# Optimization experiments

Hardware: AMD Instinct MI355X
Metric: run time of the kernel (lower is better)

## Reference

```python
import jax, jax.numpy as jnp
import numpy as np

B, D_IN = 8192, 4096
H1, H2, LAT = 2048, 1024, 256
NQ, NL = 16, 2


def setup_inputs() -> dict:
    key = jax.random.key(0)
    ks = jax.random.split(key, 16)
    def lin(k, fan_in, fan_out):
        k1, k2 = jax.random.split(k)
        s = 1.0 / np.sqrt(fan_in)
        W = jax.random.uniform(k1, (fan_out, fan_in), jnp.float32, -s, s)
        b = jax.random.uniform(k2, (fan_out,), jnp.float32, -s, s)
        return W, b
    x = jax.random.normal(ks[0], (B, D_IN), jnp.float32)
    We1, be1 = lin(ks[1], D_IN, H1)
    We2, be2 = lin(ks[2], H1, H2)
    We3, be3 = lin(ks[3], H2, LAT)
    P = jax.random.normal(ks[4], (NL, NQ, 3), jnp.float32)  # ansatz params (rx,ry,rz)
    Wd1, bd1 = lin(ks[5], NQ, H2)
    Wd2, bd2 = lin(ks[6], H2, H1)
    Wd3, bd3 = lin(ks[7], H1, D_IN)
    return {"x": x, "We1": We1, "be1": be1, "We2": We2, "be2": be2,
            "We3": We3, "be3": be3, "P": P, "Wd1": Wd1, "bd1": bd1,
            "Wd2": Wd2, "bd2": bd2, "Wd3": Wd3, "bd3": bd3}


def _quantum_block(latent, P):
    """Exact simulation of the per-qubit circuit (all gates single-qubit, so the
    2^n statevector factorizes into per-qubit 2-vectors (a,b) over |0>,|1>).
    latent: (B, LAT), P: (NL, NQ, 3). Returns Z-expectations (B, NQ)."""
    nq = P.shape[1]
    th = latent[:, :nq]  # encoding RY angles, (B, NQ)
    # RY(th)|0> = cos(th/2)|0> + sin(th/2)|1>
    a = jnp.cos(th / 2).astype(jnp.complex64)  # (B, NQ)
    b = jnp.sin(th / 2).astype(jnp.complex64)
    for l in range(P.shape[0]):
        # RX
        t = P[l, :, 0] / 2
        c, s = jnp.cos(t).astype(jnp.complex64), jnp.sin(t).astype(jnp.complex64)
        a, b = c * a - 1j * s * b, -1j * s * a + c * b
        # RY
        t = P[l, :, 1] / 2
        c, s = jnp.cos(t).astype(jnp.complex64), jnp.sin(t).astype(jnp.complex64)
        a, b = c * a - s * b, s * a + c * b
        # RZ
        t = P[l, :, 2] / 2
        ph = jnp.exp(-1j * t.astype(jnp.complex64))
        a, b = a * ph, b * jnp.conj(ph)
    z = (a.real ** 2 + a.imag ** 2) - (b.real ** 2 + b.imag ** 2)
    return z.astype(latent.dtype)


def reference(x, We1, be1, We2, be2, We3, be3, P,
              Wd1, bd1, Wd2, bd2, Wd3, bd3):
    h = jax.nn.relu(x @ We1.T + be1)
    h = jax.nn.relu(h @ We2.T + be2)
    latent = h @ We3.T + be3            # (B, LAT)
    refined = _quantum_block(latent, P)  # (B, NQ)
    h = jax.nn.relu(refined @ Wd1.T + bd1)
    h = jax.nn.relu(h @ Wd2.T + bd2)
    return h @ Wd3.T + bd3              # (B, D_IN)
```

## Files before the change

### kernel.cpp

```cpp
#include <hip/hip_runtime.h>

typedef __attribute__((ext_vector_type(8))) short bf16x8;
typedef __attribute__((ext_vector_type(4))) float f32x4;

__device__ __forceinline__ unsigned short f2bf(float f) {
    union { float f; unsigned int u; } v; v.f = f;
    unsigned int u = v.u;
    unsigned int r = (u + 0x7FFFu + ((u >> 16) & 1u)) >> 16;
    return (unsigned short)r;
}
__device__ __forceinline__ float bf2f(unsigned short b) {
    union { unsigned int u; float f; } v; v.u = ((unsigned int)b) << 16;
    return v.f;
}

#define GL16(g, l)                                                             \
    __builtin_amdgcn_global_load_lds(                                          \
        (__attribute__((address_space(1))) void*)(void*)(g),                   \
        (__attribute__((address_space(3))) void*)(void*)(l), 16, 0, 0)

#define SBAR() __builtin_amdgcn_sched_barrier(0)
#define BAR()  do { SBAR(); __builtin_amdgcn_s_barrier(); SBAR(); } while (0)

__global__ void castk(const float* __restrict__ in, unsigned short* __restrict__ out, int n4) {
    int stride = gridDim.x * blockDim.x;
    for (int i = blockIdx.x * blockDim.x + threadIdx.x; i < n4; i += stride) {
        float4 v = ((const float4*)in)[i];
        ushort4 o;
        o.x = f2bf(v.x); o.y = f2bf(v.y); o.z = f2bf(v.z); o.w = f2bf(v.w);
        ((ushort4*)out)[i] = o;
    }
}


template<int RELU, int OUT_BF16>
__global__ __launch_bounds__(512, 2) void gemm8p(
    const unsigned short* __restrict__ A,
    const unsigned short* __restrict__ Bm,
    const float* __restrict__ bias,
    void* __restrict__ Cout,
    int N, int K, int NT)
{
    __shared__ __align__(16) unsigned short lds[65536];

    const int tid  = threadIdx.x;
    const int lane = tid & 63;
    const int w    = tid >> 6;
    const int wm   = w >> 2;
    const int wn   = w & 3;
    const int bm   = blockIdx.y;
    const int bn   = blockIdx.x;

    const long arow0 = (long)bm * 256;
    const long brow0 = (long)bn * 256;

    const int  sc0 = tid,        sc1 = 512 + tid;
    const int  sr0 = sc0 >> 3,   sr1 = sc1 >> 3;
    const int  so0 = (((sc0 & 7) * 16) ^ ((sr0 & 7) << 4)) >> 1;
    const int  so1 = (((sc1 & 7) * 16) ^ ((sr1 & 7) << 4)) >> 1;
    const long soff0 = (long)sr0 * K + so0;
    const long soff1 = (long)sr1 * K + so1;
    const int  lb0 = (w * 64) * 8;
    const int  lb1 = (512 + w * 64) * 8;

    const int cl  = lane & 15;
    const int g16 = (lane >> 4) * 16;
    const int sw  = (cl & 7) << 4;
    const int cK0 = (g16 ^ sw) >> 1;
    const int cK1 = ((64 + g16) ^ sw) >> 1;
    const int arb = wm * 64 + cl;
    const int brb = wn * 32 + cl;

    f32x4  acc[2][2][4][2] = {};
    bf16x8 ar[4][2], b0r[2][2], b1r[2][2];

#define STAGE(G, growbase, t2, h, lo) do {                                     \
        int b_  = (t2) & 1;                                                    \
        int tt_ = (t2) >= NT ? (t2) - NT : (t2);                               \
        const unsigned short* gb_ = (G) + ((growbase) + (long)(h) * 128) * (long)K + (long)tt_ * 64; \
        unsigned short* lh_ = &lds[(lo) + (b_ * 2 + (h)) * 8192];              \
        GL16(gb_ + soff0, lh_ + lb0);                                          \
        GL16(gb_ + soff1, lh_ + lb1);                                          \
    } while (0)
#define STAGE_A(t2, h) STAGE(A,  arow0, t2, h, 0)
#define STAGE_B(t2, h) STAGE(Bm, brow0, t2, h, 32768)

#define READA(AR, mh, b_) do {                                                 \
        const unsigned short* ab_ = &lds[((b_) * 2 + (mh)) * 8192];            \
        _Pragma("unroll") for (int mp_ = 0; mp_ < 4; ++mp_) {                  \
            const unsigned short* rp_ = ab_ + (arb + mp_ * 16) * 64;           \
            AR[mp_][0] = *(const bf16x8*)(rp_ + cK0);                          \
            AR[mp_][1] = *(const bf16x8*)(rp_ + cK1);                          \
        }                                                                      \
    } while (0)
#define READB(BR, nh, b_) do {                                                 \
        const unsigned short* bb_ = &lds[32768 + ((b_) * 2 + (nh)) * 8192];    \
        _Pragma("unroll") for (int np_ = 0; np_ < 2; ++np_) {                  \
            const unsigned short* rp_ = bb_ + (brb + np_ * 16) * 64;           \
            BR[np_][0] = *(const bf16x8*)(rp_ + cK0);                          \
            BR[np_][1] = *(const bf16x8*)(rp_ + cK1);                          \
        }                                                                      \
    } while (0)
#define QUAD(mh, nh, AR, BR) do {                                              \
        __builtin_amdgcn_s_setprio(1);                                         \
        _Pragma("unroll") for (int mp_ = 0; mp_ < 4; ++mp_)                    \
        _Pragma("unroll") for (int np_ = 0; np_ < 2; ++np_)                    \
        _Pragma("unroll") for (int kk_ = 0; kk_ < 2; ++kk_)                    \
            acc[mh][nh][mp_][np_] = __builtin_amdgcn_mfma_f32_16x16x32_bf16(   \
                AR[mp_][kk_], BR[np_][kk_], acc[mh][nh][mp_][np_], 0, 0, 0);   \
        __builtin_amdgcn_s_setprio(0);                                         \
    } while (0)
#define VM6() do { SBAR(); asm volatile("s_waitcnt vmcnt(6)" ::: "memory"); SBAR(); } while (0)

    STAGE_B(0, 0); STAGE_A(0, 0); STAGE_B(0, 1); STAGE_A(0, 1);
    STAGE_B(1, 0); STAGE_A(1, 0); STAGE_B(1, 1);
    VM6();
    BAR();

    for (int t = 0; t < NT; ++t) {
        const int b = t & 1;
        READA(ar, 0, b);
        READB(b0r, 0, b);
        STAGE_A(t + 1, 1);
        BAR();
        QUAD(0, 0, ar, b0r);
        BAR();
        READB(b1r, 1, b);
        STAGE_B(t + 2, 0);
        BAR();
        QUAD(0, 1, ar, b1r);
        BAR();
        READA(ar, 1, b);
        STAGE_A(t + 2, 0);
        BAR();
        QUAD(1, 1, ar, b1r);
        BAR();
        STAGE_B(t + 2, 1);
        VM6();
        BAR();
        QUAD(1, 0, ar, b0r);
        BAR();
    }

    SBAR(); asm volatile("s_waitcnt vmcnt(0)" ::: "memory"); SBAR();

    const int r4 = (lane >> 4) * 4;
    float bv[2][2];
    #pragma unroll
    for (int nh = 0; nh < 2; ++nh)
        #pragma unroll
        for (int np = 0; np < 2; ++np)
            bv[nh][np] = bias[(long)bn * 256 + nh * 128 + wn * 32 + np * 16 + cl];

    #pragma unroll
    for (int mh = 0; mh < 2; ++mh)
        #pragma unroll
        for (int mp = 0; mp < 4; ++mp) {
            long grow = (long)bm * 256 + mh * 128 + wm * 64 + mp * 16 + r4;
            #pragma unroll
            for (int nh = 0; nh < 2; ++nh)
                #pragma unroll
                for (int np = 0; np < 2; ++np) {
                    long gcol = (long)bn * 256 + nh * 128 + wn * 32 + np * 16 + cl;
                    #pragma unroll
                    for (int r = 0; r < 4; ++r) {
                        float v = acc[mh][nh][mp][np][r] + bv[nh][np];
                        if (RELU) v = fmaxf(v, 0.f);
                        long idx = (grow + r) * (long)N + gcol;
                        if (OUT_BF16) ((unsigned short*)Cout)[idx] = f2bf(v);
                        else          ((float*)Cout)[idx]          = v;
                    }
                }
        }
#undef STAGE
#undef STAGE_A
#undef STAGE_B
#undef READA
#undef READB
#undef QUAD
#undef VM6
}

__global__ __launch_bounds__(256) void latq_d1(
    const unsigned short* __restrict__ h2,
    const float* __restrict__ We3,
    const float* __restrict__ be3,
    const float* __restrict__ P,
    const float* __restrict__ Wd1,
    const float* __restrict__ bd1,
    unsigned short* __restrict__ h3)
{
    __shared__ float zsh[4][16];
    const int lane = threadIdx.x & 63;
    const int wv   = threadIdx.x >> 6;
    const long row = (long)blockIdx.x * 4 + wv;

    float hreg[16];
    const unsigned short* hr = h2 + row * 1024;
    #pragma unroll
    for (int j = 0; j < 16; ++j) hreg[j] = bf2f(hr[lane + 64 * j]);

    float myth = 0.f;
    #pragma unroll
    for (int q = 0; q < 16; ++q) {
        const float* wq = We3 + q * 1024;
        float p = 0.f;
        #pragma unroll
        for (int j = 0; j < 16; ++j) p += hreg[j] * wq[lane + 64 * j];
        #pragma unroll
        for (int o = 32; o; o >>= 1) p += __shfl_xor(p, o, 64);
        if (lane == q) myth = p + be3[q];
    }

    if (lane < 16) {
        const int q = lane;
        float ar = cosf(0.5f * myth), ai = 0.f;
        float br = sinf(0.5f * myth), bi = 0.f;
        #pragma unroll
        for (int l = 0; l < 2; ++l) {
            const float* pp = P + (l * 16 + q) * 3;
            float t, c, s, ar2, ai2, br2, bi2;
            t = 0.5f * pp[0]; c = cosf(t); s = sinf(t);
            ar2 = c * ar + s * bi;  ai2 = c * ai - s * br;
            br2 = c * br + s * ai;  bi2 = c * bi - s * ar;
            ar = ar2; ai = ai2; br = br2; bi = bi2;
            t = 0.5f * pp[1]; c = cosf(t); s = sinf(t);
            ar2 = c * ar - s * br;  ai2 = c * ai - s * bi;
            br2 = s * ar + c * br;  bi2 = s * ai + c * bi;
            ar = ar2; ai = ai2; br = br2; bi = bi2;
            t = 0.5f * pp[2]; c = cosf(t); s = sinf(t);
            ar2 = ar * c + ai * s;  ai2 = ai * c - ar * s;
            br2 = br * c - bi * s;  bi2 = bi * c + br * s;
            ar = ar2; ai = ai2; br = br2; bi = bi2;
        }
        zsh[wv][q] = ar * ar + ai * ai - (br * br + bi * bi);
    }
    __syncthreads();

    float z[16];
    #pragma unroll
    for (int q = 0; q < 16; ++q) z[q] = zsh[wv][q];

    unsigned short* orow = h3 + row * 1024;
    #pragma unroll
    for (int i = 0; i < 16; ++i) {
        int j = lane + 64 * i;
        const float4* wrow = (const float4*)(Wd1 + j * 16);
        float acc = bd1[j];
        #pragma unroll
        for (int qq = 0; qq < 4; ++qq) {
            float4 w4 = wrow[qq];
            acc += z[qq * 4 + 0] * w4.x + z[qq * 4 + 1] * w4.y
                 + z[qq * 4 + 2] * w4.z + z[qq * 4 + 3] * w4.w;
        }
        orow[j] = f2bf(fmaxf(acc, 0.f));
    }
}

static void launch_cast(const float* in, unsigned short* out, long n, hipStream_t stream) {
    int n4 = (int)(n / 4);
    int blocks = (n4 + 255) / 256;
    if (blocks > 2048) blocks = 2048;
    castk<<<blocks, 256, 0, stream>>>(in, out, n4);
}

extern "C" void kernel_launch(void* const* d_in, const int* in_sizes, int n_in,
                              void* d_out, int out_size, void* d_ws, size_t ws_size,
                              hipStream_t stream) {
    const float* x   = (const float*)d_in[0];
    const float* We1 = (const float*)d_in[1];
    const float* be1 = (const float*)d_in[2];
    const float* We2 = (const float*)d_in[3];
    const float* be2 = (const float*)d_in[4];
    const float* We3 = (const float*)d_in[5];
    const float* be3 = (const float*)d_in[6];
    const float* P   = (const float*)d_in[7];
    const float* Wd1 = (const float*)d_in[8];
    const float* bd1 = (const float*)d_in[9];
    const float* Wd2 = (const float*)d_in[10];
    const float* bd2 = (const float*)d_in[11];
    const float* Wd3 = (const float*)d_in[12];
    const float* bd3 = (const float*)d_in[13];

    const int B = 8192, DIN = 4096, NH1 = 2048, NH2 = 1024;

    char* w = (char*)d_ws;
    unsigned short* x_bf   = (unsigned short*)(w);
    unsigned short* h4     = x_bf;
    unsigned short* We1_bf = (unsigned short*)(w + 67108864L);
    unsigned short* We2_bf = (unsigned short*)(w + 83886080L);
    unsigned short* Wd2_bf = (unsigned short*)(w + 88080384L);
    unsigned short* Wd3_bf = (unsigned short*)(w + 92274688L);
    unsigned short* h1     = (unsigned short*)(w + 109051904L);
    unsigned short* h3     = h1;
    unsigned short* h2     = (unsigned short*)(w + 142606336L);

    launch_cast(x,   x_bf,   (long)B * DIN,   stream);
    launch_cast(We1, We1_bf, (long)NH1 * DIN, stream);
    launch_cast(We2, We2_bf, (long)NH2 * NH1, stream);
    launch_cast(Wd2, Wd2_bf, (long)NH1 * NH2, stream);
    launch_cast(Wd3, Wd3_bf, (long)DIN * NH1, stream);

    gemm8p<1, 1><<<dim3(NH1 / 256, B / 256), 512, 0, stream>>>(x_bf, We1_bf, be1, h1, NH1, DIN, DIN >> 6);
    gemm8p<1, 1><<<dim3(NH2 / 256, B / 256), 512, 0, stream>>>(h1, We2_bf, be2, h2, NH2, NH1, NH1 >> 6);
    latq_d1<<<dim3(B / 4), 256, 0, stream>>>(h2, We3, be3, P, Wd1, bd1, h3);
    gemm8p<1, 1><<<dim3(NH1 / 256, B / 256), 512, 0, stream>>>(h3, Wd2_bf, bd2, h4, NH1, NH2, NH2 >> 6);
    gemm8p<0, 0><<<dim3(DIN / 256, B / 256), 512, 0, stream>>>(h4, Wd3_bf, bd3, d_out, DIN, NH1, NH1 >> 6);
}
```

Baseline: 451.3 us.

## Double-buffer fragment registers across iterations and stage bf16 epilogue through LDS

The GEMM main loop now keeps two sets of A and B fragment registers and prefetches the next half-tile fragments during the current MFMA quads, including loading the next k-tile's A0/B0 before the loop ends. The aim is to hide LDS read latency behind MFMA work. An extra vmcnt wait is added mid-iteration to keep this correct. The bf16 output path now writes results into LDS and then stores coalesced 16-byte rows to global, in place of scattered 2-byte stores. Staging offsets also move from 64-bit to 32-bit ints. The cost is higher register pressure and extra barriers.

```diff
diff --git a/kernel.cpp b/kernel.cpp
--- a/kernel.cpp
+++ b/kernel.cpp
@@ -54,14 +54,14 @@
     const long arow0 = (long)bm * 256;
     const long brow0 = (long)bn * 256;
 
-    const int  sc0 = tid,        sc1 = 512 + tid;
-    const int  sr0 = sc0 >> 3,   sr1 = sc1 >> 3;
-    const int  so0 = (((sc0 & 7) * 16) ^ ((sr0 & 7) << 4)) >> 1;
-    const int  so1 = (((sc1 & 7) * 16) ^ ((sr1 & 7) << 4)) >> 1;
-    const long soff0 = (long)sr0 * K + so0;
-    const long soff1 = (long)sr1 * K + so1;
-    const int  lb0 = (w * 64) * 8;
-    const int  lb1 = (512 + w * 64) * 8;
+    const int sc0 = tid,      sc1 = 512 + tid;
+    const int sr0 = sc0 >> 3, sr1 = sc1 >> 3;
+    const int so0 = (((sc0 & 7) * 16) ^ ((sr0 & 7) << 4)) >> 1;
+    const int so1 = (((sc1 & 7) * 16) ^ ((sr1 & 7) << 4)) >> 1;
+    const int soff0 = sr0 * K + so0;
+    const int soff1 = sr1 * K + so1;
+    const int lb0 = (w * 64) * 8;
+    const int lb1 = (512 + w * 64) * 8;
 
     const int cl  = lane & 15;
     const int g16 = (lane >> 4) * 16;
@@ -72,7 +72,7 @@
     const int brb = wn * 32 + cl;
 
     f32x4  acc[2][2][4][2] = {};
-    bf16x8 ar[4][2], b0r[2][2], b1r[2][2];
+    bf16x8 a0[4][2], a1[4][2], b0[2][2], b1[2][2];
 
 #define STAGE(G, growbase, t2, h, lo) do {                                     \
         int b_  = (t2) & 1;                                                    \
@@ -116,33 +116,37 @@
     STAGE_B(1, 0); STAGE_A(1, 0); STAGE_B(1, 1);
     VM6();
     BAR();
+    READA(a0, 0, 0);
+    READB(b0, 0, 0);
 
     for (int t = 0; t < NT; ++t) {
         const int b = t & 1;
-        READA(ar, 0, b);
-        READB(b0r, 0, b);
+        READA(a1, 1, b);
         STAGE_A(t + 1, 1);
         BAR();
-        QUAD(0, 0, ar, b0r);
-        BAR();
-        READB(b1r, 1, b);
+        QUAD(0, 0, a0, b0);
+        BAR();
+        READB(b1, 1, b);
         STAGE_B(t + 2, 0);
-        BAR();
-        QUAD(0, 1, ar, b1r);
-        BAR();
-        READA(ar, 1, b);
+        VM6();
+        BAR();
+        QUAD(0, 1, a0, b1);
+        BAR();
+        READA(a0, 0, b ^ 1);
         STAGE_A(t + 2, 0);
         BAR();
-        QUAD(1, 1, ar, b1r);
+        QUAD(1, 1, a1, b1);
         BAR();
         STAGE_B(t + 2, 1);
         VM6();
         BAR();
-        QUAD(1, 0, ar, b0r);
+        QUAD(1, 0, a1, b0);
+        READB(b0, 0, b ^ 1);
         BAR();
     }
 
     SBAR(); asm volatile("s_waitcnt vmcnt(0)" ::: "memory"); SBAR();
+    BAR();
 
     const int r4 = (lane >> 4) * 4;
     float bv[2][2];
@@ -152,26 +156,55 @@
         for (int np = 0; np < 2; ++np)
             bv[nh][np] = bias[(long)bn * 256 + nh * 128 + wn * 32 + np * 16 + cl];
 
-    #pragma unroll
-    for (int mh = 0; mh < 2; ++mh)
-        #pragma unroll
-        for (int mp = 0; mp < 4; ++mp) {
-            long grow = (long)bm * 256 + mh * 128 + wm * 64 + mp * 16 + r4;
+    if (OUT_BF16) {
+        unsigned short* epi = lds;
+        #pragma unroll
+        for (int h = 0; h < 2; ++h) {
+            if (h) BAR();
             #pragma unroll
-            for (int nh = 0; nh < 2; ++nh)
+            for (int mp = 0; mp < 4; ++mp)
                 #pragma unroll
-                for (int np = 0; np < 2; ++np) {
-                    long gcol = (long)bn * 256 + nh * 128 + wn * 32 + np * 16 + cl;
+                for (int nh = 0; nh < 2; ++nh)
                     #pragma unroll
-                    for (int r = 0; r < 4; ++r) {
-                        float v = acc[mh][nh][mp][np][r] + bv[nh][np];
-                        if (RELU) v = fmaxf(v, 0.f);
-                        long idx = (grow + r) * (long)N + gcol;
-                        if (OUT_BF16) ((unsigned short*)Cout)[idx] = f2bf(v);
-                        else          ((float*)Cout)[idx]          = v;
+                    for (int np = 0; np < 2; ++np)
+                        #pragma unroll
+                        for (int r = 0; r < 4; ++r) {
+                            float v = acc[h][nh][mp][np][r] + bv[nh][np];
+                            if (RELU) v = fmaxf(v, 0.f);
+                            int lrow = wm * 64 + mp * 16 + r4 + r;
+                            int lcol = nh * 128 + wn * 32 + np * 16 + cl;
+                            epi[lrow * 264 + lcol] = f2bf(v);
+                        }
+            BAR();
+            long rowg0 = (long)bm * 256 + h * 128;
+            #pragma unroll
+            for (int i = 0; i < 8; ++i) {
+                int row = (tid >> 5) + i * 16;
+                int cc  = (tid & 31) * 8;
+                bf16x8 v8 = *(const bf16x8*)&epi[row * 264 + cc];
+                *(bf16x8*)((unsigned short*)Cout + (rowg0 + row) * (long)N + (long)bn * 256 + cc) = v8;
+            }
+        }
+    } else {
+        #pragma unroll
+        for (int mh = 0; mh < 2; ++mh)
+            #pragma unroll
+            for (int mp = 0; mp < 4; ++mp) {
+                long grow = (long)bm * 256 + mh * 128 + wm * 64 + mp * 16 + r4;
+                #pragma unroll
+                for (int nh = 0; nh < 2; ++nh)
+                    #pragma unroll
+                    for (int np = 0; np < 2; ++np) {
+                        long gcol = (long)bn * 256 + nh * 128 + wn * 32 + np * 16 + cl;
+                        #pragma unroll
+                        for (int r = 0; r < 4; ++r) {
+                            float v = acc[mh][nh][mp][np][r] + bv[nh][np];
+                            if (RELU) v = fmaxf(v, 0.f);
+                            ((float*)Cout)[(grow + r) * (long)N + gcol] = v;
+                        }
                     }
-                }
-        }
+            }
+    }
 #undef STAGE
 #undef STAGE_A
 #undef STAGE_B
```

Measured after the change: 441.8 us. 2.1% less time.
